# Performance work log

Measured on AMD Instinct MI355X. Metric: run time of the kernel, lower is better.

The kernel has to match this reference:

```python
import jax, jax.numpy as jnp
import numpy as np

N = 50000          # nodes (multiple of p+e=8)
E = 400000         # edges (avg degree 8)
H, C = 4, 128      # heads, per-head channels
IN = 5             # input node feature dim
HID = 512          # mlp hidden dim
P, EV = 4, 4       # pursuers / evaders per graph
NEG_SLOPE = 0.2    # GATConv leaky_relu slope

# static team index: nodes with idx % (P+EV) < P  (team='pursuer')
_idx = np.arange(N)
TEAM_IDX = jnp.asarray(_idx[_idx % (P + EV) < P])  # [N/2]


def setup_inputs() -> dict:
    key = jax.random.key(0)
    ks = jax.random.split(key, 16)
    s = 0.1
    return {
        "x": jax.random.normal(ks[0], (N, IN), jnp.float32),
        "edge_index": jax.random.randint(ks[1], (2, E), 0, N, jnp.int64),
        "edge_attr": jax.random.normal(ks[2], (E, 2), jnp.float32),
        # GATConv params
        "W": jax.random.normal(ks[3], (H * C, IN), jnp.float32) * s,
        "att_src": jax.random.normal(ks[4], (H, C), jnp.float32) * s,
        "att_dst": jax.random.normal(ks[5], (H, C), jnp.float32) * s,
        "bias": jnp.zeros((H * C,), jnp.float32),
        # MLP head params
        "W1": jax.random.normal(ks[6], (HID, H * C), jnp.float32) * s,
        "b1": jnp.zeros((HID,), jnp.float32),
        "W2": jax.random.normal(ks[7], (HID, HID), jnp.float32) * s,
        "b2": jnp.zeros((HID,), jnp.float32),
        "W3": jax.random.normal(ks[8], (2, HID), jnp.float32) * s,
        "b3": jnp.zeros((2,), jnp.float32),
    }


def _gat_max(x, src, dst, W, att_src, att_dst, bias):
    # linear transform: [N, H, C]
    h = (x @ W.T).reshape(N, H, C)
    a_src = jnp.einsum("nhc,hc->nh", h, att_src)  # [N, H]
    a_dst = jnp.einsum("nhc,hc->nh", h, att_dst)  # [N, H]
    # per-edge attention logits, leaky relu
    alpha = jax.nn.leaky_relu(a_src[src] + a_dst[dst], NEG_SLOPE)  # [Et, H]
    # segment softmax over incoming edges of each dst node
    amax = jax.ops.segment_max(alpha, dst, num_segments=N)  # [N, H]
    ex = jnp.exp(alpha - amax[dst])
    den = jax.ops.segment_sum(ex, dst, num_segments=N)      # [N, H]
    attn = ex / den[dst]                                     # [Et, H]
    # alpha-weighted messages, scatter-MAX aggregation (aggr='max')
    msg = h[src] * attn[:, :, None]                          # [Et, H, C]
    out = jax.ops.segment_max(msg, dst, num_segments=N)     # [N, H, C]
    return out.reshape(N, H * C) + bias


def reference(x, edge_index, edge_attr, W, att_src, att_dst, bias,
              W1, b1, W2, b2, W3, b3):
    # PyG GATConv default add_self_loops=True; edge_attr ignored (edge_dim=None)
    loops = jnp.arange(N, dtype=edge_index.dtype)
    src = jnp.concatenate([edge_index[0], loops])
    dst = jnp.concatenate([edge_index[1], loops])
    emb = _gat_max(x, src, dst, W, att_src, att_dst, bias)  # [N, 512]
    h = emb[TEAM_IDX]                                        # [N/2, 512]
    h = jax.nn.relu(h @ W1.T + b1)
    h = jax.nn.relu(h @ W2.T + b2)
    return jnp.tanh(h @ W3.T + b3)                           # [N/2, 2]
```

## Files before the change

### kernel.cpp

```cpp
#include <hip/hip_runtime.h>
#include <hip/hip_bf16.h>
#include <math.h>

#define N_NODES 50000
#define N_EDGES 400000
#define HEADS   4
#define HC      512
#define IN_DIM  5
#define M_SEL   25000
#define NEG_SLOPE 0.2f

typedef __attribute__((ext_vector_type(8))) short bf16x8;
typedef __attribute__((ext_vector_type(4))) float f32x4;

__device__ inline unsigned short f2bf(float f) {
    union { float f; unsigned u; } v; v.f = f;
    unsigned r = v.u + 0x7FFF + ((v.u >> 16) & 1);
    return (unsigned short)(r >> 16);
}
__device__ inline float bf2f(unsigned short b) {
    union { unsigned u; float f; } v; v.u = ((unsigned)b) << 16;
    return v.f;
}

__global__ void k_cvt2(const float* __restrict__ W1, const float* __restrict__ W2,
                       unsigned short* __restrict__ W1b, unsigned short* __restrict__ W2b) {
    int i = blockIdx.x * 256 + threadIdx.x;
    const float* src = (i < 65536) ? W1 : W2;
    unsigned short* dst = (i < 65536) ? W1b : W2b;
    int j = i & 65535;
    float4 v = ((const float4*)src)[j];
    ushort4 o;
    o.x = f2bf(v.x); o.y = f2bf(v.y); o.z = f2bf(v.z); o.w = f2bf(v.w);
    ((ushort4*)dst)[j] = o;
}

#define TR_NPW 8

__global__ __launch_bounds__(256) void k_transform(
        const float* __restrict__ x, const float* __restrict__ W,
        const float* __restrict__ att_src, const float* __restrict__ att_dst,
        unsigned short* __restrict__ h, float* __restrict__ a_src,
        float* __restrict__ a_dst, int* __restrict__ deg) {
    int wave = threadIdx.x >> 6, lane = threadIdx.x & 63;
    int c0 = lane * 8;

    float wreg[40];
    const float4* wp = (const float4*)(W + c0 * IN_DIM);
#pragma unroll
    for (int i = 0; i < 10; i++) ((float4*)wreg)[i] = wp[i];
    float sas[8], sad[8];
    *(float4*)&sas[0] = *(const float4*)(att_src + c0);
    *(float4*)&sas[4] = *(const float4*)(att_src + c0 + 4);
    *(float4*)&sad[0] = *(const float4*)(att_dst + c0);
    *(float4*)&sad[4] = *(const float4*)(att_dst + c0 + 4);

    int n0 = (blockIdx.x * 4 + wave) * TR_NPW;
#pragma unroll
    for (int t = 0; t < TR_NPW; t++) {
        int n = n0 + t;
        if (n >= N_NODES) return;
        float xv[IN_DIM];
#pragma unroll
        for (int i = 0; i < IN_DIM; i++) xv[i] = x[n * IN_DIM + i];

        float ps = 0.f, pd = 0.f;
        bf16x8 hv8;
#pragma unroll
        for (int j = 0; j < 8; j++) {
            float acc = 0.f;
#pragma unroll
            for (int i = 0; i < IN_DIM; i++) acc += xv[i] * wreg[j * IN_DIM + i];
            hv8[j] = (short)f2bf(acc);
            ps += acc * sas[j];
            pd += acc * sad[j];
        }
        *(bf16x8*)(h + (size_t)n * HC + c0) = hv8;

#pragma unroll
        for (int off = 8; off >= 1; off >>= 1) {
            ps += __shfl_xor(ps, off);
            pd += __shfl_xor(pd, off);
        }
        if ((lane & 15) == 0) {
            int head = lane >> 4;
            a_src[n * HEADS + head] = ps;
            a_dst[n * HEADS + head] = pd;
        }
        if (lane == 0) deg[n] = 1;
    }
}

__global__ void k_hist(const int* __restrict__ ei, int* __restrict__ deg) {
    int e = blockIdx.x * 256 + threadIdx.x;
    if (e < N_EDGES) atomicAdd(&deg[ei[N_EDGES + e]], 1);
}

__global__ void k_scan1(const int* __restrict__ deg, int* __restrict__ excl,
                        int* __restrict__ bsum) {
    __shared__ int s[256];
    int i = blockIdx.x * 256 + threadIdx.x;
    int v = (i < N_NODES) ? deg[i] : 0;
    s[threadIdx.x] = v;
    __syncthreads();
    for (int off = 1; off < 256; off <<= 1) {
        int t = (threadIdx.x >= off) ? s[threadIdx.x - off] : 0;
        __syncthreads();
        s[threadIdx.x] += t;
        __syncthreads();
    }
    if (i < N_NODES) excl[i] = s[threadIdx.x] - v;
    if (threadIdx.x == 255) bsum[blockIdx.x] = s[255];
}

__global__ void k_scan2(int* __restrict__ bsum, int nb) {
    if (threadIdx.x == 0 && blockIdx.x == 0) {
        int acc = 0;
        for (int b = 0; b < nb; b++) { int v = bsum[b]; bsum[b] = acc; acc += v; }
    }
}

__global__ void k_scan3fill(int* __restrict__ excl, const int* __restrict__ bsum,
                            int* __restrict__ offs, int* __restrict__ curs,
                            int* __restrict__ csr) {
    int i = blockIdx.x * 256 + threadIdx.x;
    if (i < N_NODES) {
        int o = excl[i] + bsum[blockIdx.x];
        offs[i] = o;
        csr[o] = i;
        curs[i] = o + 1;
    }
}

__global__ void k_fill_edges(const int* __restrict__ ei, int* __restrict__ cursor,
                             int* __restrict__ csr) {
    int e = blockIdx.x * 256 + threadIdx.x;
    if (e < N_EDGES) {
        int d = ei[N_EDGES + e];
        int pos = atomicAdd(&cursor[d], 1);
        csr[pos] = ei[e];
    }
}

__global__ void k_aggregate(const unsigned short* __restrict__ h, const float* __restrict__ a_src,
                            const float* __restrict__ a_dst, const int* __restrict__ csr,
                            const int* __restrict__ offs, const int* __restrict__ deg,
                            const float* __restrict__ bias, unsigned short* __restrict__ emb_sel) {
    int wave = threadIdx.x >> 6, lane = threadIdx.x & 63;
    int w = blockIdx.x * 4 + wave;
    if (w >= M_SEL) return;
    int n = ((w >> 2) << 3) + (w & 3);

    int base = offs[n];
    int dn = deg[n];
    int head = lane >> 4, egrp = lane & 15;
    float adn = a_dst[n * HEADS + head];
    int c0 = lane * 8;

    float acc[8];
#pragma unroll
    for (int j = 0; j < 8; j++) acc[j] = -INFINITY;

    if (dn <= 16) {
        int s_e = 0;
        float t = -INFINITY;
        if (egrp < dn) {
            s_e = csr[base + egrp];
            t = a_src[s_e * HEADS + head] + adn;
            t = (t > 0.f) ? t : NEG_SLOPE * t;
        }
        float m = t;
#pragma unroll
        for (int off = 8; off >= 1; off >>= 1) m = fmaxf(m, __shfl_xor(m, off));
        float ex = (egrp < dn) ? __expf(t - m) : 0.f;
        float den = ex;
#pragma unroll
        for (int off = 8; off >= 1; off >>= 1) den += __shfl_xor(den, off);
        float attn = ex / den;

        int e = 0;
        for (; e + 4 <= dn; e += 4) {
            int s0 = __shfl(s_e, e + 0), s1 = __shfl(s_e, e + 1);
            int s2 = __shfl(s_e, e + 2), s3 = __shfl(s_e, e + 3);
            float a0 = __shfl(attn, (head << 4) | (e + 0));
            float a1 = __shfl(attn, (head << 4) | (e + 1));
            float a2 = __shfl(attn, (head << 4) | (e + 2));
            float a3 = __shfl(attn, (head << 4) | (e + 3));
            bf16x8 v0 = *(const bf16x8*)(h + (size_t)s0 * HC + c0);
            bf16x8 v1 = *(const bf16x8*)(h + (size_t)s1 * HC + c0);
            bf16x8 v2 = *(const bf16x8*)(h + (size_t)s2 * HC + c0);
            bf16x8 v3 = *(const bf16x8*)(h + (size_t)s3 * HC + c0);
#pragma unroll
            for (int j = 0; j < 8; j++) {
                acc[j] = fmaxf(acc[j], bf2f((unsigned short)v0[j]) * a0);
                acc[j] = fmaxf(acc[j], bf2f((unsigned short)v1[j]) * a1);
                acc[j] = fmaxf(acc[j], bf2f((unsigned short)v2[j]) * a2);
                acc[j] = fmaxf(acc[j], bf2f((unsigned short)v3[j]) * a3);
            }
        }
        for (; e < dn; e++) {
            int s = __shfl(s_e, e);
            float a = __shfl(attn, (head << 4) | e);
            bf16x8 v = *(const bf16x8*)(h + (size_t)s * HC + c0);
#pragma unroll
            for (int j = 0; j < 8; j++)
                acc[j] = fmaxf(acc[j], bf2f((unsigned short)v[j]) * a);
        }
    } else {
        float m = -INFINITY;
        for (int e0 = 0; e0 < dn; e0 += 16) {
            int e = e0 + egrp;
            if (e < dn) {
                int s = csr[base + e];
                float t = a_src[s * HEADS + head] + adn;
                t = (t > 0.f) ? t : NEG_SLOPE * t;
                m = fmaxf(m, t);
            }
        }
#pragma unroll
        for (int off = 8; off >= 1; off >>= 1) m = fmaxf(m, __shfl_xor(m, off));
        float den = 0.f;
        for (int e0 = 0; e0 < dn; e0 += 16) {
            int e = e0 + egrp;
            if (e < dn) {
                int s = csr[base + e];
                float t = a_src[s * HEADS + head] + adn;
                t = (t > 0.f) ? t : NEG_SLOPE * t;
                den += __expf(t - m);
            }
        }
#pragma unroll
        for (int off = 8; off >= 1; off >>= 1) den += __shfl_xor(den, off);
        float invden = 1.0f / den;
        for (int e = 0; e < dn; e++) {
            int s = csr[base + e];
            float t = a_src[s * HEADS + head] + adn;
            t = (t > 0.f) ? t : NEG_SLOPE * t;
            float attn = __expf(t - m) * invden;
            bf16x8 hv = *(const bf16x8*)(h + (size_t)s * HC + c0);
#pragma unroll
            for (int j = 0; j < 8; j++)
                acc[j] = fmaxf(acc[j], bf2f((unsigned short)hv[j]) * attn);
        }
    }

    bf16x8 ov;
#pragma unroll
    for (int j = 0; j < 8; j++) ov[j] = (short)f2bf(acc[j] + bias[c0 + j]);
    *(bf16x8*)(emb_sel + (size_t)w * HC + c0) = ov;
}

#define BK  64
#define LDK 72

template <bool RELU>
__global__ __launch_bounds__(512, 2) void k_gemm(const unsigned short* __restrict__ A, int M,
                                                 const unsigned short* __restrict__ Wt,
                                                 const float* __restrict__ bias,
                                                 unsigned short* __restrict__ C) {
    __shared__ unsigned short As[256 * LDK];
    __shared__ unsigned short Bs[256 * LDK];
    int tid = threadIdx.x;
    int m0 = blockIdx.y * 256;
    int o0 = blockIdx.x * 256;
    int wv = tid >> 6, lane = tid & 63;
    int wm = wv >> 1, wn = wv & 1;

    f32x4 acc[4][8];
#pragma unroll
    for (int i = 0; i < 4; i++)
#pragma unroll
        for (int j = 0; j < 8; j++) acc[i][j] = (f32x4){0.f, 0.f, 0.f, 0.f};

    bf16x8 ra[4], rb[4];
#pragma unroll
    for (int s = 0; s < 4; s++) {
        int c = s * 512 + tid;
        int row = c >> 3, col = (c & 7) * 8;
        int m = m0 + row;
        bf16x8 av = {0, 0, 0, 0, 0, 0, 0, 0};
        if (m < M) av = *(const bf16x8*)(A + (size_t)m * HC + col);
        ra[s] = av;
        rb[s] = *(const bf16x8*)(Wt + (size_t)(o0 + row) * HC + col);
    }

    for (int k0 = 0; k0 < HC; k0 += BK) {
        __syncthreads();
#pragma unroll
        for (int s = 0; s < 4; s++) {
            int c = s * 512 + tid;
            int row = c >> 3, col = (c & 7) * 8;
            *(bf16x8*)(&As[row * LDK + col]) = ra[s];
            *(bf16x8*)(&Bs[row * LDK + col]) = rb[s];
        }
        __syncthreads();

        int kn = k0 + BK;
        if (kn < HC) {
#pragma unroll
            for (int s = 0; s < 4; s++) {
                int c = s * 512 + tid;
                int row = c >> 3, col = (c & 7) * 8;
                int m = m0 + row;
                bf16x8 av = {0, 0, 0, 0, 0, 0, 0, 0};
                if (m < M) av = *(const bf16x8*)(A + (size_t)m * HC + kn + col);
                ra[s] = av;
                rb[s] = *(const bf16x8*)(Wt + (size_t)(o0 + row) * HC + kn + col);
            }
        }

#pragma unroll
        for (int kk = 0; kk < 2; kk++) {
            int kb = kk * 32 + (lane >> 4) * 8;
            bf16x8 af[4], bfr[8];
#pragma unroll
            for (int mi = 0; mi < 4; mi++)
                af[mi] = *(const bf16x8*)(&As[(wm * 64 + mi * 16 + (lane & 15)) * LDK + kb]);
#pragma unroll
            for (int ni = 0; ni < 8; ni++)
                bfr[ni] = *(const bf16x8*)(&Bs[(wn * 128 + ni * 16 + (lane & 15)) * LDK + kb]);
#pragma unroll
            for (int mi = 0; mi < 4; mi++)
#pragma unroll
                for (int ni = 0; ni < 8; ni++)
                    acc[mi][ni] = __builtin_amdgcn_mfma_f32_16x16x32_bf16(
                        af[mi], bfr[ni], acc[mi][ni], 0, 0, 0);
        }
    }

#pragma unroll
    for (int ni = 0; ni < 8; ni++) {
        int ncol = o0 + wn * 128 + ni * 16 + (lane & 15);
        float bv = bias[ncol];
#pragma unroll
        for (int mi = 0; mi < 4; mi++) {
            int mbase = m0 + wm * 64 + mi * 16 + (lane >> 4) * 4;
#pragma unroll
            for (int r = 0; r < 4; r++) {
                int m = mbase + r;
                if (m < M) {
                    float v = acc[mi][ni][r] + bv;
                    if (RELU) v = fmaxf(v, 0.f);
                    C[(size_t)m * HC + ncol] = f2bf(v);
                }
            }
        }
    }
}

__global__ void k_final(const unsigned short* __restrict__ h2, const float* __restrict__ W3,
                        const float* __restrict__ b3, float* __restrict__ out, int M) {
    int wave = threadIdx.x >> 6, lane = threadIdx.x & 63;
    int m = blockIdx.x * 4 + wave;
    if (m >= M) return;
    float s0 = 0.f, s1 = 0.f;
    bf16x8 hv = *(const bf16x8*)(h2 + (size_t)m * HC + lane * 8);
#pragma unroll
    for (int j = 0; j < 8; j++) {
        int k = lane * 8 + j;
        float v = bf2f((unsigned short)hv[j]);
        s0 += v * W3[k];
        s1 += v * W3[HC + k];
    }
#pragma unroll
    for (int off = 32; off >= 1; off >>= 1) {
        s0 += __shfl_xor(s0, off);
        s1 += __shfl_xor(s1, off);
    }
    if (lane == 0) {
        out[(size_t)m * 2 + 0] = tanhf(s0 + b3[0]);
        out[(size_t)m * 2 + 1] = tanhf(s1 + b3[1]);
    }
}

extern "C" void kernel_launch(void* const* d_in, const int* in_sizes, int n_in,
                              void* d_out, int out_size, void* d_ws, size_t ws_size,
                              hipStream_t stream) {
    const float* x       = (const float*)d_in[0];
    const int*   ei      = (const int*)d_in[1];
    const float* W       = (const float*)d_in[3];
    const float* att_src = (const float*)d_in[4];
    const float* att_dst = (const float*)d_in[5];
    const float* bias    = (const float*)d_in[6];
    const float* W1      = (const float*)d_in[7];
    const float* b1      = (const float*)d_in[8];
    const float* W2      = (const float*)d_in[9];
    const float* b2      = (const float*)d_in[10];
    const float* W3      = (const float*)d_in[11];
    const float* b3      = (const float*)d_in[12];
    float* out = (float*)d_out;

    char* ws = (char*)d_ws;
    unsigned short* h       = (unsigned short*)(ws);
    unsigned short* emb_sel = (unsigned short*)(ws + 51200000);
    unsigned short* h1      = (unsigned short*)(ws + 76800000);
    unsigned short* h2      = (unsigned short*)(ws + 102400000);
    unsigned short* W1b     = (unsigned short*)(ws + 128000000);
    unsigned short* W2b     = (unsigned short*)(ws + 128524288);
    float* a_src = (float*)(ws + 129048576);
    float* a_dst = (float*)(ws + 129848576);
    int*   deg   = (int*)  (ws + 130648576);
    int*   offs  = (int*)  (ws + 130848576);
    int*   curs  = (int*)  (ws + 131048576);
    int*   excl  = (int*)  (ws + 131248576);
    int*   bsum  = (int*)  (ws + 131448576);
    int*   csr   = (int*)  (ws + 131449600);

    k_cvt2<<<512, 256, 0, stream>>>(W1, W2, W1b, W2b);
    k_transform<<<(N_NODES + 31) / 32, 256, 0, stream>>>(x, W, att_src, att_dst, h,
                                                         a_src, a_dst, deg);
    k_hist<<<(N_EDGES + 255) / 256, 256, 0, stream>>>(ei, deg);
    k_scan1<<<196, 256, 0, stream>>>(deg, excl, bsum);
    k_scan2<<<1, 64, 0, stream>>>(bsum, 196);
    k_scan3fill<<<196, 256, 0, stream>>>(excl, bsum, offs, curs, csr);
    k_fill_edges<<<(N_EDGES + 255) / 256, 256, 0, stream>>>(ei, curs, csr);
    k_aggregate<<<6250, 256, 0, stream>>>(h, a_src, a_dst, csr, offs, deg, bias, emb_sel);

    dim3 g(2, 98);
    k_gemm<true><<<g, 512, 0, stream>>>(emb_sel, M_SEL, W1b, b1, h1);
    k_gemm<true><<<g, 512, 0, stream>>>(h1, M_SEL, W2b, b2, h2);
    k_final<<<(M_SEL + 3) / 4, 256, 0, stream>>>(h2, W3, b3, out, M_SEL);
}
```

Before: 216.1 us.

## Drop weight-convert and serial scan kernels; batch neighbor gathers in aggregation

Removes the separate fp32-to-bf16 weight conversion kernel by converting W1/W2 tiles to bf16 inside the GEMM load path. It also folds the single-thread block-sum scan into k_scan3fill, where each block rescans the 196 partial sums in shared memory. The aggregation kernel now issues all up-to-16 neighbor row loads before the softmax so memory latency overlaps the attention math. The trade-offs are higher register use for 16 buffered vectors, twice the weight bytes read per GEMM tile, and redundant scan work in every block.

```diff
diff --git a/kernel.cpp b/kernel.cpp
--- a/kernel.cpp
+++ b/kernel.cpp
@@ -23,18 +23,6 @@
     return v.f;
 }
 
-__global__ void k_cvt2(const float* __restrict__ W1, const float* __restrict__ W2,
-                       unsigned short* __restrict__ W1b, unsigned short* __restrict__ W2b) {
-    int i = blockIdx.x * 256 + threadIdx.x;
-    const float* src = (i < 65536) ? W1 : W2;
-    unsigned short* dst = (i < 65536) ? W1b : W2b;
-    int j = i & 65535;
-    float4 v = ((const float4*)src)[j];
-    ushort4 o;
-    o.x = f2bf(v.x); o.y = f2bf(v.y); o.z = f2bf(v.z); o.w = f2bf(v.w);
-    ((ushort4*)dst)[j] = o;
-}
-
 #define TR_NPW 8
 
 __global__ __launch_bounds__(256) void k_transform(
@@ -95,6 +83,8 @@
     int e = blockIdx.x * 256 + threadIdx.x;
     if (e < N_EDGES) atomicAdd(&deg[ei[N_EDGES + e]], 1);
 }
+
+#define NSCAN_BLK 196
 
 __global__ void k_scan1(const int* __restrict__ deg, int* __restrict__ excl,
                         int* __restrict__ bsum) {
@@ -113,19 +103,23 @@
     if (threadIdx.x == 255) bsum[blockIdx.x] = s[255];
 }
 
-__global__ void k_scan2(int* __restrict__ bsum, int nb) {
-    if (threadIdx.x == 0 && blockIdx.x == 0) {
-        int acc = 0;
-        for (int b = 0; b < nb; b++) { int v = bsum[b]; bsum[b] = acc; acc += v; }
-    }
-}
-
-__global__ void k_scan3fill(int* __restrict__ excl, const int* __restrict__ bsum,
+__global__ void k_scan3fill(const int* __restrict__ excl, const int* __restrict__ bsum,
                             int* __restrict__ offs, int* __restrict__ curs,
                             int* __restrict__ csr) {
-    int i = blockIdx.x * 256 + threadIdx.x;
+    __shared__ int part[256];
+    int tid = threadIdx.x;
+    part[tid] = (tid < NSCAN_BLK) ? bsum[tid] : 0;
+    __syncthreads();
+    for (int off = 1; off < 256; off <<= 1) {
+        int t = (tid >= off) ? part[tid - off] : 0;
+        __syncthreads();
+        part[tid] += t;
+        __syncthreads();
+    }
+    int blockoff = (blockIdx.x == 0) ? 0 : part[blockIdx.x - 1];
+    int i = blockIdx.x * 256 + tid;
     if (i < N_NODES) {
-        int o = excl[i] + bsum[blockIdx.x];
+        int o = excl[i] + blockoff;
         offs[i] = o;
         csr[o] = i;
         curs[i] = o + 1;
@@ -154,7 +148,6 @@
     int base = offs[n];
     int dn = deg[n];
     int head = lane >> 4, egrp = lane & 15;
-    float adn = a_dst[n * HEADS + head];
     int c0 = lane * 8;
 
     float acc[8];
@@ -163,9 +156,20 @@
 
     if (dn <= 16) {
         int s_e = 0;
+        if (egrp < dn) s_e = csr[base + egrp];
+
+        bf16x8 v[16];
+#pragma unroll
+        for (int e = 0; e < 16; e++) {
+            if (e < dn) {
+                int s = __shfl(s_e, e);
+                v[e] = *(const bf16x8*)(h + (size_t)s * HC + c0);
+            }
+        }
+
+        float adn = a_dst[n * HEADS + head];
         float t = -INFINITY;
         if (egrp < dn) {
-            s_e = csr[base + egrp];
             t = a_src[s_e * HEADS + head] + adn;
             t = (t > 0.f) ? t : NEG_SLOPE * t;
         }
@@ -178,35 +182,17 @@
         for (int off = 8; off >= 1; off >>= 1) den += __shfl_xor(den, off);
         float attn = ex / den;
 
-        int e = 0;
-        for (; e + 4 <= dn; e += 4) {
-            int s0 = __shfl(s_e, e + 0), s1 = __shfl(s_e, e + 1);
-            int s2 = __shfl(s_e, e + 2), s3 = __shfl(s_e, e + 3);
-            float a0 = __shfl(attn, (head << 4) | (e + 0));
-            float a1 = __shfl(attn, (head << 4) | (e + 1));
-            float a2 = __shfl(attn, (head << 4) | (e + 2));
-            float a3 = __shfl(attn, (head << 4) | (e + 3));
-            bf16x8 v0 = *(const bf16x8*)(h + (size_t)s0 * HC + c0);
-            bf16x8 v1 = *(const bf16x8*)(h + (size_t)s1 * HC + c0);
-            bf16x8 v2 = *(const bf16x8*)(h + (size_t)s2 * HC + c0);
-            bf16x8 v3 = *(const bf16x8*)(h + (size_t)s3 * HC + c0);
-#pragma unroll
-            for (int j = 0; j < 8; j++) {
-                acc[j] = fmaxf(acc[j], bf2f((unsigned short)v0[j]) * a0);
-                acc[j] = fmaxf(acc[j], bf2f((unsigned short)v1[j]) * a1);
-                acc[j] = fmaxf(acc[j], bf2f((unsigned short)v2[j]) * a2);
-                acc[j] = fmaxf(acc[j], bf2f((unsigned short)v3[j]) * a3);
-            }
-        }
-        for (; e < dn; e++) {
-            int s = __shfl(s_e, e);
-            float a = __shfl(attn, (head << 4) | e);
-            bf16x8 v = *(const bf16x8*)(h + (size_t)s * HC + c0);
-#pragma unroll
-            for (int j = 0; j < 8; j++)
-                acc[j] = fmaxf(acc[j], bf2f((unsigned short)v[j]) * a);
+#pragma unroll
+        for (int e = 0; e < 16; e++) {
+            if (e < dn) {
+                float a = __shfl(attn, (head << 4) | e);
+#pragma unroll
+                for (int j = 0; j < 8; j++)
+                    acc[j] = fmaxf(acc[j], bf2f((unsigned short)v[e][j]) * a);
+            }
         }
     } else {
+        float adn = a_dst[n * HEADS + head];
         float m = -INFINITY;
         for (int e0 = 0; e0 < dn; e0 += 16) {
             int e = e0 + egrp;
@@ -253,9 +239,18 @@
 #define BK  64
 #define LDK 72
 
+__device__ inline bf16x8 cvt8(float4 a, float4 b) {
+    bf16x8 r;
+    r[0] = (short)f2bf(a.x); r[1] = (short)f2bf(a.y);
+    r[2] = (short)f2bf(a.z); r[3] = (short)f2bf(a.w);
+    r[4] = (short)f2bf(b.x); r[5] = (short)f2bf(b.y);
+    r[6] = (short)f2bf(b.z); r[7] = (short)f2bf(b.w);
+    return r;
+}
+
 template <bool RELU>
 __global__ __launch_bounds__(512, 2) void k_gemm(const unsigned short* __restrict__ A, int M,
-                                                 const unsigned short* __restrict__ Wt,
+                                                 const float* __restrict__ Wt,
                                                  const float* __restrict__ bias,
                                                  unsigned short* __restrict__ C) {
     __shared__ unsigned short As[256 * LDK];
@@ -281,7 +276,8 @@
         bf16x8 av = {0, 0, 0, 0, 0, 0, 0, 0};
         if (m < M) av = *(const bf16x8*)(A + (size_t)m * HC + col);
         ra[s] = av;
-        rb[s] = *(const bf16x8*)(Wt + (size_t)(o0 + row) * HC + col);
+        const float4* wp = (const float4*)(Wt + (size_t)(o0 + row) * HC + col);
+        rb[s] = cvt8(wp[0], wp[1]);
     }
 
     for (int k0 = 0; k0 < HC; k0 += BK) {
@@ -305,7 +301,8 @@
                 bf16x8 av = {0, 0, 0, 0, 0, 0, 0, 0};
                 if (m < M) av = *(const bf16x8*)(A + (size_t)m * HC + kn + col);
                 ra[s] = av;
-                rb[s] = *(const bf16x8*)(Wt + (size_t)(o0 + row) * HC + kn + col);
+                const float4* wp = (const float4*)(Wt + (size_t)(o0 + row) * HC + kn + col);
+                rb[s] = cvt8(wp[0], wp[1]);
             }
         }
 
@@ -395,8 +392,6 @@
     unsigned short* emb_sel = (unsigned short*)(ws + 51200000);
     unsigned short* h1      = (unsigned short*)(ws + 76800000);
     unsigned short* h2      = (unsigned short*)(ws + 102400000);
-    unsigned short* W1b     = (unsigned short*)(ws + 128000000);
-    unsigned short* W2b     = (unsigned short*)(ws + 128524288);
     float* a_src = (float*)(ws + 129048576);
     float* a_dst = (float*)(ws + 129848576);
     int*   deg   = (int*)  (ws + 130648576);
@@ -406,18 +401,16 @@
     int*   bsum  = (int*)  (ws + 131448576);
     int*   csr   = (int*)  (ws + 131449600);
 
-    k_cvt2<<<512, 256, 0, stream>>>(W1, W2, W1b, W2b);
     k_transform<<<(N_NODES + 31) / 32, 256, 0, stream>>>(x, W, att_src, att_dst, h,
                                                          a_src, a_dst, deg);
     k_hist<<<(N_EDGES + 255) / 256, 256, 0, stream>>>(ei, deg);
-    k_scan1<<<196, 256, 0, stream>>>(deg, excl, bsum);
-    k_scan2<<<1, 64, 0, stream>>>(bsum, 196);
-    k_scan3fill<<<196, 256, 0, stream>>>(excl, bsum, offs, curs, csr);
+    k_scan1<<<NSCAN_BLK, 256, 0, stream>>>(deg, excl, bsum);
+    k_scan3fill<<<NSCAN_BLK, 256, 0, stream>>>(excl, bsum, offs, curs, csr);
     k_fill_edges<<<(N_EDGES + 255) / 256, 256, 0, stream>>>(ei, curs, csr);
     k_aggregate<<<6250, 256, 0, stream>>>(h, a_src, a_dst, csr, offs, deg, bias, emb_sel);
 
     dim3 g(2, 98);
-    k_gemm<true><<<g, 512, 0, stream>>>(emb_sel, M_SEL, W1b, b1, h1);
-    k_gemm<true><<<g, 512, 0, stream>>>(h1, M_SEL, W2b, b2, h2);
+    k_gemm<true><<<g, 512, 0, stream>>>(emb_sel, M_SEL, W1, b1, h1);
+    k_gemm<true><<<g, 512, 0, stream>>>(h1, M_SEL, W2, b2, h2);
     k_final<<<(M_SEL + 3) / 4, 256, 0, stream>>>(h2, W3, b3, out, M_SEL);
 }
```

Measured after the change: 208.8 us. 3.4% less time.
